# Optimization experiments

Hardware: AMD Instinct MI355X
Metric: run time of the kernel (lower is better)

## Reference

```python
import jax, jax.numpy as jnp
import numpy as np

B, D, O = 512, 256, 256
H = [512, 1024, 1024]

def _linear_params(key, fan_in, fan_out):
    kw, kb = jax.random.split(key)
    bound = 1.0 / np.sqrt(fan_in)
    W = jax.random.uniform(kw, (fan_out, fan_in), jnp.float32, -bound, bound)
    b = jax.random.uniform(kb, (fan_out,), jnp.float32, -bound, bound)
    return W, b

def setup_inputs() -> dict:
    key = jax.random.key(0)
    ks = jax.random.split(key, 7)
    input_values = jax.random.normal(ks[0], (B, D), jnp.float32)
    nan_flag = jax.random.uniform(ks[1], (B, D), jnp.float32)
    W_in, b_in = _linear_params(ks[2], D, H[0])          # input_layer: nan_flag_dim -> H[0]
    W_h1, b_h1 = _linear_params(ks[3], H[0], H[1])        # hidden layer 1
    W_h2, b_h2 = _linear_params(ks[4], H[1], H[2])        # hidden layer 2
    W_d, b_d = _linear_params(ks[5], H[2], D * O)         # output_branch_dense
    W_b, b_b = _linear_params(ks[6], H[2], O)             # output_branch_bias
    return {"input_values": input_values, "nan_flag": nan_flag, "training": False,
            "W_in": W_in, "b_in": b_in, "W_h1": W_h1, "b_h1": b_h1,
            "W_h2": W_h2, "b_h2": b_h2, "W_d": W_d, "b_d": b_d,
            "W_b": W_b, "b_b": b_b}

def reference(input_values, nan_flag, training, W_in, b_in, W_h1, b_h1, W_h2, b_h2, W_d, b_d, W_b, b_b):
    # training=False: dropout is identity, sample_missing branch skipped (default False)
    x = jax.nn.relu(nan_flag @ W_in.T + b_in)
    x = jax.nn.relu(x @ W_h1.T + b_h1)
    x = jax.nn.relu(x @ W_h2.T + b_h2)
    # per-sample compensation weights [B, D, O] and bias [B, O]
    comp_w = (x @ W_d.T + b_d).reshape(B, D, O)
    comp_b = x @ W_b.T + b_b
    # baddbmm: [B,1,D] @ [B,D,O] + [B,1,O] -> squeeze -> [B,O]
    out = comp_b + jnp.einsum('bd,bdo->bo', input_values, comp_w)
    return out
```

## Files before the change

kernel.cpp:

```cpp
#include <hip/hip_runtime.h>
#include <hip/hip_bf16.h>

#define B_  512
#define D_  256
#define O_  256
#define H2_ 1024

typedef __attribute__((ext_vector_type(4))) float  f32x4;
typedef __attribute__((ext_vector_type(8))) short  short8;
typedef __attribute__((ext_vector_type(4))) short  short4v;

union S8u  { short4v v; unsigned u[2]; };
union S16u { short8  v; unsigned u[4]; };

__device__ __forceinline__ unsigned f32_bf16(float x) {
  unsigned u = __builtin_bit_cast(unsigned, x);
  return (u + 0x7fffu + ((u >> 16) & 1u)) >> 16;
}
__device__ __forceinline__ unsigned cvt_pk_bf16(float a, float b) {
  return f32_bf16(a) | (f32_bf16(b) << 16);
}

__device__ __forceinline__ void gl_lds16(const void* g, void* l) {
  __builtin_amdgcn_global_load_lds(
      (const __attribute__((address_space(1))) unsigned int*)g,
      (__attribute__((address_space(3))) unsigned int*)l, 16, 0, 0);
}

__global__ __launch_bounds__(256)
void wcvt(const float* __restrict__ src, ushort* __restrict__ dst, int n8) {
  int i = blockIdx.x * 256 + threadIdx.x;
  const int stride = gridDim.x * 256;
  for (; i < n8; i += stride) {
    const f32x4* p = (const f32x4*)(src + (size_t)i * 8);
    f32x4 a = p[0], b = p[1];
    S16u s;
    s.u[0] = cvt_pk_bf16(a.x, a.y);
    s.u[1] = cvt_pk_bf16(a.z, a.w);
    s.u[2] = cvt_pk_bf16(b.x, b.y);
    s.u[3] = cvt_pk_bf16(b.z, b.w);
    *(short8*)(dst + (size_t)i * 8) = s.v;
  }
}

template <int RELU>
__global__ __launch_bounds__(256)
void gemm_bt64(const float* __restrict__ A, const float* __restrict__ Bm,
               const float* __restrict__ bias, float* __restrict__ C,
               int M, int N, int K) {
  __shared__ __align__(16) short As[64][72];
  __shared__ __align__(16) short Bs[64][72];
  const int t    = threadIdx.x;
  const int m0   = blockIdx.y * 64;
  const int n0   = blockIdx.x * 64;
  const int f4c  = t & 15;
  const int rg   = t >> 4;
  const int lane = t & 63;
  const int w    = t >> 6;
  const int wm   = (w & 1) * 32;
  const int wn   = (w >> 1) * 32;
  const int lr   = lane & 15;
  const int lq   = lane >> 4;

  f32x4 acc[2][2];
  #pragma unroll
  for (int i = 0; i < 2; ++i)
    #pragma unroll
    for (int j = 0; j < 2; ++j) acc[i][j] = f32x4{0.f, 0.f, 0.f, 0.f};

  for (int k0 = 0; k0 < K; k0 += 64) {
    #pragma unroll
    for (int j = 0; j < 4; ++j) {
      int r = rg + 16 * j;
      f32x4 av = *(const f32x4*)(A  + (size_t)(m0 + r) * K + k0 + f4c * 4);
      f32x4 bv = *(const f32x4*)(Bm + (size_t)(n0 + r) * K + k0 + f4c * 4);
      S8u sa; sa.u[0] = cvt_pk_bf16(av.x, av.y); sa.u[1] = cvt_pk_bf16(av.z, av.w);
      S8u sb; sb.u[0] = cvt_pk_bf16(bv.x, bv.y); sb.u[1] = cvt_pk_bf16(bv.z, bv.w);
      *(short4v*)&As[r][f4c * 4] = sa.v;
      *(short4v*)&Bs[r][f4c * 4] = sb.v;
    }
    __syncthreads();
    #pragma unroll
    for (int ks = 0; ks < 2; ++ks) {
      short8 a0 = *(const short8*)&As[wm + lr     ][ks * 32 + lq * 8];
      short8 a1 = *(const short8*)&As[wm + 16 + lr][ks * 32 + lq * 8];
      short8 b0 = *(const short8*)&Bs[wn + lr     ][ks * 32 + lq * 8];
      short8 b1 = *(const short8*)&Bs[wn + 16 + lr][ks * 32 + lq * 8];
      acc[0][0] = __builtin_amdgcn_mfma_f32_16x16x32_bf16(a0, b0, acc[0][0], 0, 0, 0);
      acc[0][1] = __builtin_amdgcn_mfma_f32_16x16x32_bf16(a0, b1, acc[0][1], 0, 0, 0);
      acc[1][0] = __builtin_amdgcn_mfma_f32_16x16x32_bf16(a1, b0, acc[1][0], 0, 0, 0);
      acc[1][1] = __builtin_amdgcn_mfma_f32_16x16x32_bf16(a1, b1, acc[1][1], 0, 0, 0);
    }
    __syncthreads();
  }
  #pragma unroll
  for (int mi = 0; mi < 2; ++mi)
    #pragma unroll
    for (int ni = 0; ni < 2; ++ni)
      #pragma unroll
      for (int r = 0; r < 4; ++r) {
        int row = m0 + wm + mi * 16 + lq * 4 + r;
        int col = n0 + wn + ni * 16 + lr;
        float v = acc[mi][ni][r] + bias[col];
        if (RELU) v = fmaxf(v, 0.f);
        C[(size_t)row * N + col] = v;
      }
}

__global__ __launch_bounds__(256)
void bias_d_kernel(const float* __restrict__ inp, const float* __restrict__ b_d,
                   float* __restrict__ out) {
  const int b = blockIdx.x;
  const int o = threadIdx.x;
  const float* ir = inp + (size_t)b * D_;
  float s = 0.f;
  #pragma unroll 8
  for (int d = 0; d < D_; ++d)
    s += ir[d] * b_d[(size_t)d * O_ + o];
  out[(size_t)b * O_ + o] += s;
}

__global__ __launch_bounds__(256)
void stage_b3(const float* __restrict__ x2, const float* __restrict__ inp,
              const ushort* __restrict__ Wdb, float* __restrict__ out) {
  __shared__ __align__(16) short  As[128][72];
  __shared__ __align__(16) ushort Bs[128 * 64];
  const int t    = threadIdx.x;
  const int mt   = blockIdx.x >> 1;
  const int nt   = blockIdx.x & 1;
  const int d0   = blockIdx.y * 4;
  const int bm   = mt * 128;
  const int bn   = nt * 128;
  const int f4c  = t & 15;
  const int rg   = t >> 4;
  const int lane = t & 63;
  const int w    = t >> 6;
  const int wm   = (w & 1) * 64;
  const int wn   = (w >> 1) * 64;
  const int lr   = lane & 15;
  const int lq   = lane >> 4;
  const int srow = t >> 3;
  const int skc  = (t & 7) ^ ((t >> 3) & 7);

  f32x4 acc[4][4];
  #pragma unroll
  for (int mi = 0; mi < 4; ++mi)
    #pragma unroll
    for (int ni = 0; ni < 4; ++ni) acc[mi][ni] = f32x4{0.f, 0.f, 0.f, 0.f};

  for (int dl = 0; dl < 4; ++dl) {
    const int d = d0 + dl;
    float insc[8];
    #pragma unroll
    for (int j = 0; j < 8; ++j)
      insc[j] = inp[(size_t)(bm + rg + 16 * j) * D_ + d];
    const ushort* wb = Wdb + ((size_t)d * O_ + bn) * H2_;

    for (int h0 = 0; h0 < H2_; h0 += 64) {
      #pragma unroll
      for (int r = 0; r < 4; ++r) {
        int n = r * 32 + srow;
        gl_lds16(wb + (size_t)n * H2_ + h0 + skc * 8, &Bs[(size_t)(r * 256 + t) * 8]);
      }
      #pragma unroll
      for (int j = 0; j < 8; ++j) {
        int rrow = rg + 16 * j;
        f32x4 xv = *(const f32x4*)(x2 + (size_t)(bm + rrow) * H2_ + h0 + f4c * 4);
        float s = insc[j];
        S8u sa;
        sa.u[0] = cvt_pk_bf16(xv.x * s, xv.y * s);
        sa.u[1] = cvt_pk_bf16(xv.z * s, xv.w * s);
        *(short4v*)&As[rrow][f4c * 4] = sa.v;
      }
      __syncthreads();
      #pragma unroll
      for (int ks = 0; ks < 2; ++ks) {
        short8 af[4], bfr[4];
        #pragma unroll
        for (int mi = 0; mi < 4; ++mi)
          af[mi] = *(const short8*)&As[wm + mi * 16 + lr][ks * 32 + lq * 8];
        #pragma unroll
        for (int ni = 0; ni < 4; ++ni) {
          int n  = wn + ni * 16 + lr;
          int kc = (ks * 4 + lq) ^ (n & 7);
          bfr[ni] = *(const short8*)&Bs[(size_t)(n * 8 + kc) * 8];
        }
        #pragma unroll
        for (int mi = 0; mi < 4; ++mi)
          #pragma unroll
          for (int ni = 0; ni < 4; ++ni)
            acc[mi][ni] = __builtin_amdgcn_mfma_f32_16x16x32_bf16(af[mi], bfr[ni],
                                                                  acc[mi][ni], 0, 0, 0);
      }
      __syncthreads();
    }
  }

  #pragma unroll
  for (int mi = 0; mi < 4; ++mi)
    #pragma unroll
    for (int ni = 0; ni < 4; ++ni)
      #pragma unroll
      for (int r = 0; r < 4; ++r) {
        int row = bm + wm + mi * 16 + lq * 4 + r;
        int col = bn + wn + ni * 16 + lr;
        atomicAdd(out + (size_t)row * O_ + col, acc[mi][ni][r]);
      }
}

__global__ __launch_bounds__(256, 2)
void stage_b(const float* __restrict__ x2, const float* __restrict__ inp,
             const float* __restrict__ Wd, float* __restrict__ out) {
  __shared__ __align__(16) short As[128][72];
  __shared__ __align__(16) short Bs[128][72];
  const int t    = threadIdx.x;
  const int mt   = blockIdx.x >> 1;
  const int nt   = blockIdx.x & 1;
  const int d0   = blockIdx.y * 4;
  const int bm   = mt * 128;
  const int bn   = nt * 128;
  const int f4c  = t & 15;
  const int rg   = t >> 4;
  const int lane = t & 63;
  const int w    = t >> 6;
  const int wm   = (w & 1) * 64;
  const int wn   = (w >> 1) * 64;
  const int lr   = lane & 15;
  const int lq   = lane >> 4;

  f32x4 acc[4][4];
  #pragma unroll
  for (int mi = 0; mi < 4; ++mi)
    #pragma unroll
    for (int ni = 0; ni < 4; ++ni) acc[mi][ni] = f32x4{0.f, 0.f, 0.f, 0.f};

  for (int dl = 0; dl < 4; ++dl) {
    const int d = d0 + dl;
    float insc[8];
    #pragma unroll
    for (int j = 0; j < 8; ++j)
      insc[j] = inp[(size_t)(bm + rg + 16 * j) * D_ + d];
    const float* wbase = Wd + ((size_t)d * O_ + bn) * H2_;

    for (int h0 = 0; h0 < H2_; h0 += 64) {
      #pragma unroll
      for (int j = 0; j < 8; ++j) {
        int r = rg + 16 * j;
        f32x4 xv = *(const f32x4*)(x2 + (size_t)(bm + r) * H2_ + h0 + f4c * 4);
        float s = insc[j];
        S8u sa;
        sa.u[0] = cvt_pk_bf16(xv.x * s, xv.y * s);
        sa.u[1] = cvt_pk_bf16(xv.z * s, xv.w * s);
        *(short4v*)&As[r][f4c * 4] = sa.v;
        f32x4 wv = *(const f32x4*)(wbase + (size_t)r * H2_ + h0 + f4c * 4);
        S8u sb; sb.u[0] = cvt_pk_bf16(wv.x, wv.y); sb.u[1] = cvt_pk_bf16(wv.z, wv.w);
        *(short4v*)&Bs[r][f4c * 4] = sb.v;
      }
      __syncthreads();
      #pragma unroll
      for (int ks = 0; ks < 2; ++ks) {
        short8 af[4], bfr[4];
        #pragma unroll
        for (int mi = 0; mi < 4; ++mi)
          af[mi] = *(const short8*)&As[wm + mi * 16 + lr][ks * 32 + lq * 8];
        #pragma unroll
        for (int ni = 0; ni < 4; ++ni)
          bfr[ni] = *(const short8*)&Bs[wn + ni * 16 + lr][ks * 32 + lq * 8];
        #pragma unroll
        for (int mi = 0; mi < 4; ++mi)
          #pragma unroll
          for (int ni = 0; ni < 4; ++ni)
            acc[mi][ni] = __builtin_amdgcn_mfma_f32_16x16x32_bf16(af[mi], bfr[ni],
                                                                  acc[mi][ni], 0, 0, 0);
      }
      __syncthreads();
    }
  }

  #pragma unroll
  for (int mi = 0; mi < 4; ++mi)
    #pragma unroll
    for (int ni = 0; ni < 4; ++ni)
      #pragma unroll
      for (int r = 0; r < 4; ++r) {
        int row = bm + wm + mi * 16 + lq * 4 + r;
        int col = bn + wn + ni * 16 + lr;
        atomicAdd(out + (size_t)row * O_ + col, acc[mi][ni][r]);
      }
}

extern "C" void kernel_launch(void* const* d_in, const int* in_sizes, int n_in,
                              void* d_out, int out_size, void* d_ws, size_t ws_size,
                              hipStream_t stream) {
  const float* input = (const float*)d_in[0];
  const float* nanf  = (const float*)d_in[1];
  const float* W_in  = (const float*)d_in[3];
  const float* b_in  = (const float*)d_in[4];
  const float* W_h1  = (const float*)d_in[5];
  const float* b_h1  = (const float*)d_in[6];
  const float* W_h2  = (const float*)d_in[7];
  const float* b_h2  = (const float*)d_in[8];
  const float* W_d   = (const float*)d_in[9];
  const float* b_d   = (const float*)d_in[10];
  const float* W_b   = (const float*)d_in[11];
  const float* b_b   = (const float*)d_in[12];
  float* out = (float*)d_out;

  float* x0 = (float*)d_ws;
  float* x1 = x0 + 512 * 512;
  float* x2 = x1 + 512 * 1024;
  ushort* Wdb = (ushort*)(x2 + 512 * 1024);
  const size_t need = 5242880 + (size_t)65536 * 1024 * 2;
  const bool use_bf16_w = ws_size >= need;

  if (use_bf16_w)
    wcvt<<<8192, 256, 0, stream>>>(W_d, Wdb, 65536 * 1024 / 8);

  gemm_bt64<1><<<dim3(8, 8),  256, 0, stream>>>(nanf, W_in, b_in, x0, 512, 512, 256);
  gemm_bt64<1><<<dim3(16, 8), 256, 0, stream>>>(x0, W_h1, b_h1, x1, 512, 1024, 512);
  gemm_bt64<1><<<dim3(16, 8), 256, 0, stream>>>(x1, W_h2, b_h2, x2, 512, 1024, 1024);
  gemm_bt64<0><<<dim3(4, 8),  256, 0, stream>>>(x2, W_b, b_b, out, 512, 256, 1024);
  bias_d_kernel<<<512, 256, 0, stream>>>(input, b_d, out);

  if (use_bf16_w)
    stage_b3<<<dim3(8, 64), 256, 0, stream>>>(x2, input, Wdb, out);
  else
    stage_b<<<dim3(8, 64), 256, 0, stream>>>(x2, input, W_d, out);
}
```

Before: 645.0 us.

## Double-buffer W_d tiles in LDS and build A fragments directly from global

The main compensation-weight GEMM now double-buffers the bf16 W_d tile in shared memory, prefetching the next tile while MFMAs run on the current one, and needs only one barrier per iteration. The A operand (x2 scaled by the input value) is no longer staged through LDS. Each wave loads its fp32 rows straight from global memory, scales them, converts to bf16 in registers and feeds the MFMA. This removes the LDS A tile and a barrier per step, but adds redundant global loads of x2 across waves and more register pressure.

```diff
diff --git a/kernel.cpp b/kernel.cpp
--- a/kernel.cpp
+++ b/kernel.cpp
@@ -121,18 +121,15 @@
 }
 
 __global__ __launch_bounds__(256)
-void stage_b3(const float* __restrict__ x2, const float* __restrict__ inp,
+void stage_b5(const float* __restrict__ x2, const float* __restrict__ inp,
               const ushort* __restrict__ Wdb, float* __restrict__ out) {
-  __shared__ __align__(16) short  As[128][72];
-  __shared__ __align__(16) ushort Bs[128 * 64];
+  __shared__ __align__(16) ushort Bb[2][128 * 64];
   const int t    = threadIdx.x;
   const int mt   = blockIdx.x >> 1;
   const int nt   = blockIdx.x & 1;
   const int d0   = blockIdx.y * 4;
   const int bm   = mt * 128;
   const int bn   = nt * 128;
-  const int f4c  = t & 15;
-  const int rg   = t >> 4;
   const int lane = t & 63;
   const int w    = t >> 6;
   const int wm   = (w & 1) * 64;
@@ -148,51 +145,70 @@
     #pragma unroll
     for (int ni = 0; ni < 4; ++ni) acc[mi][ni] = f32x4{0.f, 0.f, 0.f, 0.f};
 
-  for (int dl = 0; dl < 4; ++dl) {
-    const int d = d0 + dl;
-    float insc[8];
-    #pragma unroll
-    for (int j = 0; j < 8; ++j)
-      insc[j] = inp[(size_t)(bm + rg + 16 * j) * D_ + d];
-    const ushort* wb = Wdb + ((size_t)d * O_ + bn) * H2_;
-
-    for (int h0 = 0; h0 < H2_; h0 += 64) {
+  {
+    const ushort* wb = Wdb + ((size_t)d0 * O_ + bn) * H2_;
+    #pragma unroll
+    for (int r = 0; r < 4; ++r) {
+      int n = r * 32 + srow;
+      gl_lds16(wb + (size_t)n * H2_ + skc * 8, &Bb[0][(size_t)(r * 256 + t) * 8]);
+    }
+  }
+
+  float insc[4];
+  for (int it = 0; it < 64; ++it) {
+    const int p  = it & 1;
+    const int d  = d0 + (it >> 4);
+    const int h0 = (it & 15) * 64;
+    if ((it & 15) == 0) {
+      #pragma unroll
+      for (int mi = 0; mi < 4; ++mi)
+        insc[mi] = inp[(size_t)(bm + wm + mi * 16 + lr) * D_ + d];
+    }
+    __syncthreads();
+    if (it < 63) {
+      const int itn = it + 1;
+      const int dn  = d0 + (itn >> 4);
+      const int hn  = (itn & 15) * 64;
+      const ushort* wbn = Wdb + ((size_t)dn * O_ + bn) * H2_;
       #pragma unroll
       for (int r = 0; r < 4; ++r) {
         int n = r * 32 + srow;
-        gl_lds16(wb + (size_t)n * H2_ + h0 + skc * 8, &Bs[(size_t)(r * 256 + t) * 8]);
-      }
-      #pragma unroll
-      for (int j = 0; j < 8; ++j) {
-        int rrow = rg + 16 * j;
-        f32x4 xv = *(const f32x4*)(x2 + (size_t)(bm + rrow) * H2_ + h0 + f4c * 4);
-        float s = insc[j];
-        S8u sa;
-        sa.u[0] = cvt_pk_bf16(xv.x * s, xv.y * s);
-        sa.u[1] = cvt_pk_bf16(xv.z * s, xv.w * s);
-        *(short4v*)&As[rrow][f4c * 4] = sa.v;
-      }
-      __syncthreads();
-      #pragma unroll
-      for (int ks = 0; ks < 2; ++ks) {
-        short8 af[4], bfr[4];
-        #pragma unroll
-        for (int mi = 0; mi < 4; ++mi)
-          af[mi] = *(const short8*)&As[wm + mi * 16 + lr][ks * 32 + lq * 8];
+        gl_lds16(wbn + (size_t)n * H2_ + hn + skc * 8,
+                 &Bb[1 - p][(size_t)(r * 256 + t) * 8]);
+      }
+    }
+    #pragma unroll
+    for (int ks = 0; ks < 2; ++ks) {
+      short8 bfr[4];
+      #pragma unroll
+      for (int ni = 0; ni < 4; ++ni) {
+        int n  = wn + ni * 16 + lr;
+        int kc = (ks * 4 + lq) ^ (n & 7);
+        bfr[ni] = *(const short8*)&Bb[p][(size_t)(n * 8 + kc) * 8];
+      }
+      #pragma unroll
+      for (int mh = 0; mh < 2; ++mh) {
+        const int m0i = mh * 2;
+        const float* xp0 = x2 + (size_t)(bm + wm + m0i * 16 + lr) * H2_ + h0 + ks * 32 + lq * 8;
+        const float* xp1 = x2 + (size_t)(bm + wm + (m0i + 1) * 16 + lr) * H2_ + h0 + ks * 32 + lq * 8;
+        f32x4 x0a = *(const f32x4*)xp0, x0b = *(const f32x4*)(xp0 + 4);
+        f32x4 x1a = *(const f32x4*)xp1, x1b = *(const f32x4*)(xp1 + 4);
+        float s0 = insc[m0i], s1 = insc[m0i + 1];
+        S16u a0, a1;
+        a0.u[0] = cvt_pk_bf16(x0a.x * s0, x0a.y * s0);
+        a0.u[1] = cvt_pk_bf16(x0a.z * s0, x0a.w * s0);
+        a0.u[2] = cvt_pk_bf16(x0b.x * s0, x0b.y * s0);
+        a0.u[3] = cvt_pk_bf16(x0b.z * s0, x0b.w * s0);
+        a1.u[0] = cvt_pk_bf16(x1a.x * s1, x1a.y * s1);
+        a1.u[1] = cvt_pk_bf16(x1a.z * s1, x1a.w * s1);
+        a1.u[2] = cvt_pk_bf16(x1b.x * s1, x1b.y * s1);
+        a1.u[3] = cvt_pk_bf16(x1b.z * s1, x1b.w * s1);
         #pragma unroll
         for (int ni = 0; ni < 4; ++ni) {
-          int n  = wn + ni * 16 + lr;
-          int kc = (ks * 4 + lq) ^ (n & 7);
-          bfr[ni] = *(const short8*)&Bs[(size_t)(n * 8 + kc) * 8];
+          acc[m0i][ni]     = __builtin_amdgcn_mfma_f32_16x16x32_bf16(a0.v, bfr[ni], acc[m0i][ni],     0, 0, 0);
+          acc[m0i + 1][ni] = __builtin_amdgcn_mfma_f32_16x16x32_bf16(a1.v, bfr[ni], acc[m0i + 1][ni], 0, 0, 0);
         }
-        #pragma unroll
-        for (int mi = 0; mi < 4; ++mi)
-          #pragma unroll
-          for (int ni = 0; ni < 4; ++ni)
-            acc[mi][ni] = __builtin_amdgcn_mfma_f32_16x16x32_bf16(af[mi], bfr[ni],
-                                                                  acc[mi][ni], 0, 0, 0);
-      }
-      __syncthreads();
+      }
     }
   }
 
@@ -323,7 +339,7 @@
   bias_d_kernel<<<512, 256, 0, stream>>>(input, b_d, out);
 
   if (use_bf16_w)
-    stage_b3<<<dim3(8, 64), 256, 0, stream>>>(x2, input, Wdb, out);
+    stage_b5<<<dim3(8, 64), 256, 0, stream>>>(x2, input, Wdb, out);
   else
     stage_b<<<dim3(8, 64), 256, 0, stream>>>(x2, input, W_d, out);
 }
```

Result: slower. 793.2 us (+23.0%).

## Switch main contraction to fp16 with async LDS loads of pre-converted activations

Applied to the files above, without the earlier changes.

Converts W_d and x2 to fp16 in the workspace instead of bf16. The main kernel now loads the x2 tile straight into LDS with global_load_lds and applies the per-row input scale in registers before an fp16 MFMA. This removes the per-iteration fp32 global loads, scaling and bf16 packing from the inner loop. It adds an extra conversion kernel, a larger workspace requirement, and fp16 range/precision limits on the scaled activations.

```diff
diff --git a/kernel.cpp b/kernel.cpp
--- a/kernel.cpp
+++ b/kernel.cpp
@@ -6,12 +6,13 @@
 #define O_  256
 #define H2_ 1024
 
-typedef __attribute__((ext_vector_type(4))) float  f32x4;
-typedef __attribute__((ext_vector_type(8))) short  short8;
-typedef __attribute__((ext_vector_type(4))) short  short4v;
+typedef __attribute__((ext_vector_type(4))) float    f32x4;
+typedef __attribute__((ext_vector_type(8))) short    short8;
+typedef __attribute__((ext_vector_type(4))) short    short4v;
+typedef __attribute__((ext_vector_type(8))) _Float16 half8;
 
 union S8u  { short4v v; unsigned u[2]; };
-union S16u { short8  v; unsigned u[4]; };
+union H8u  { half8 v; short8 s; };
 
 __device__ __forceinline__ unsigned f32_bf16(float x) {
   unsigned u = __builtin_bit_cast(unsigned, x);
@@ -28,18 +29,16 @@
 }
 
 __global__ __launch_bounds__(256)
-void wcvt(const float* __restrict__ src, ushort* __restrict__ dst, int n8) {
+void wcvt_h(const float* __restrict__ src, _Float16* __restrict__ dst, int n8) {
   int i = blockIdx.x * 256 + threadIdx.x;
   const int stride = gridDim.x * 256;
   for (; i < n8; i += stride) {
     const f32x4* p = (const f32x4*)(src + (size_t)i * 8);
     f32x4 a = p[0], b = p[1];
-    S16u s;
-    s.u[0] = cvt_pk_bf16(a.x, a.y);
-    s.u[1] = cvt_pk_bf16(a.z, a.w);
-    s.u[2] = cvt_pk_bf16(b.x, b.y);
-    s.u[3] = cvt_pk_bf16(b.z, b.w);
-    *(short8*)(dst + (size_t)i * 8) = s.v;
+    half8 h;
+    h[0] = (_Float16)a.x; h[1] = (_Float16)a.y; h[2] = (_Float16)a.z; h[3] = (_Float16)a.w;
+    h[4] = (_Float16)b.x; h[5] = (_Float16)b.y; h[6] = (_Float16)b.z; h[7] = (_Float16)b.w;
+    *(half8*)(dst + (size_t)i * 8) = h;
   }
 }
 
@@ -121,9 +120,9 @@
 }
 
 __global__ __launch_bounds__(256)
-void stage_b3(const float* __restrict__ x2, const float* __restrict__ inp,
-              const ushort* __restrict__ Wdb, float* __restrict__ out) {
-  __shared__ __align__(16) short  As[128][72];
+void stage_b6(const _Float16* __restrict__ x2h, const float* __restrict__ inp,
+              const _Float16* __restrict__ Wdh, float* __restrict__ out) {
+  __shared__ __align__(16) ushort As[128 * 64];
   __shared__ __align__(16) ushort Bs[128 * 64];
   const int t    = threadIdx.x;
   const int mt   = blockIdx.x >> 1;
@@ -131,8 +130,6 @@
   const int d0   = blockIdx.y * 4;
   const int bm   = mt * 128;
   const int bn   = nt * 128;
-  const int f4c  = t & 15;
-  const int rg   = t >> 4;
   const int lane = t & 63;
   const int w    = t >> 6;
   const int wm   = (w & 1) * 64;
@@ -148,49 +145,47 @@
     #pragma unroll
     for (int ni = 0; ni < 4; ++ni) acc[mi][ni] = f32x4{0.f, 0.f, 0.f, 0.f};
 
+  const _Float16* xa = x2h + (size_t)bm * H2_;
+
   for (int dl = 0; dl < 4; ++dl) {
     const int d = d0 + dl;
-    float insc[8];
-    #pragma unroll
-    for (int j = 0; j < 8; ++j)
-      insc[j] = inp[(size_t)(bm + rg + 16 * j) * D_ + d];
-    const ushort* wb = Wdb + ((size_t)d * O_ + bn) * H2_;
+    const _Float16* wb = Wdh + ((size_t)d * O_ + bn) * H2_;
+    _Float16 hs[4];
+    #pragma unroll
+    for (int mi = 0; mi < 4; ++mi)
+      hs[mi] = (_Float16)inp[(size_t)(bm + wm + mi * 16 + lr) * D_ + d];
 
     for (int h0 = 0; h0 < H2_; h0 += 64) {
       #pragma unroll
       for (int r = 0; r < 4; ++r) {
         int n = r * 32 + srow;
+        gl_lds16(xa + (size_t)n * H2_ + h0 + skc * 8, &As[(size_t)(r * 256 + t) * 8]);
         gl_lds16(wb + (size_t)n * H2_ + h0 + skc * 8, &Bs[(size_t)(r * 256 + t) * 8]);
       }
-      #pragma unroll
-      for (int j = 0; j < 8; ++j) {
-        int rrow = rg + 16 * j;
-        f32x4 xv = *(const f32x4*)(x2 + (size_t)(bm + rrow) * H2_ + h0 + f4c * 4);
-        float s = insc[j];
-        S8u sa;
-        sa.u[0] = cvt_pk_bf16(xv.x * s, xv.y * s);
-        sa.u[1] = cvt_pk_bf16(xv.z * s, xv.w * s);
-        *(short4v*)&As[rrow][f4c * 4] = sa.v;
-      }
       __syncthreads();
       #pragma unroll
       for (int ks = 0; ks < 2; ++ks) {
-        short8 af[4], bfr[4];
-        #pragma unroll
-        for (int mi = 0; mi < 4; ++mi)
-          af[mi] = *(const short8*)&As[wm + mi * 16 + lr][ks * 32 + lq * 8];
+        half8 af[4], bfr[4];
+        #pragma unroll
+        for (int mi = 0; mi < 4; ++mi) {
+          int m  = wm + mi * 16 + lr;
+          int kc = (ks * 4 + lq) ^ (lr & 7);
+          af[mi] = *(const half8*)&As[(size_t)(m * 8 + kc) * 8];
+        }
         #pragma unroll
         for (int ni = 0; ni < 4; ++ni) {
           int n  = wn + ni * 16 + lr;
-          int kc = (ks * 4 + lq) ^ (n & 7);
-          bfr[ni] = *(const short8*)&Bs[(size_t)(n * 8 + kc) * 8];
+          int kc = (ks * 4 + lq) ^ (lr & 7);
+          bfr[ni] = *(const half8*)&Bs[(size_t)(n * 8 + kc) * 8];
         }
         #pragma unroll
-        for (int mi = 0; mi < 4; ++mi)
+        for (int mi = 0; mi < 4; ++mi) {
+          half8 asb = af[mi] * hs[mi];
           #pragma unroll
           for (int ni = 0; ni < 4; ++ni)
-            acc[mi][ni] = __builtin_amdgcn_mfma_f32_16x16x32_bf16(af[mi], bfr[ni],
-                                                                  acc[mi][ni], 0, 0, 0);
+            acc[mi][ni] = __builtin_amdgcn_mfma_f32_16x16x32_f16(asb, bfr[ni],
+                                                                 acc[mi][ni], 0, 0, 0);
+        }
       }
       __syncthreads();
     }
@@ -309,12 +304,13 @@
   float* x0 = (float*)d_ws;
   float* x1 = x0 + 512 * 512;
   float* x2 = x1 + 512 * 1024;
-  ushort* Wdb = (ushort*)(x2 + 512 * 1024);
-  const size_t need = 5242880 + (size_t)65536 * 1024 * 2;
-  const bool use_bf16_w = ws_size >= need;
-
-  if (use_bf16_w)
-    wcvt<<<8192, 256, 0, stream>>>(W_d, Wdb, 65536 * 1024 / 8);
+  _Float16* Wdh = (_Float16*)(x2 + 512 * 1024);
+  _Float16* x2h = Wdh + (size_t)65536 * 1024;
+  const size_t need = 5242880 + ((size_t)65536 * 1024 + 512 * 1024) * 2;
+  const bool use_f16 = ws_size >= need;
+
+  if (use_f16)
+    wcvt_h<<<8192, 256, 0, stream>>>(W_d, Wdh, 65536 * 1024 / 8);
 
   gemm_bt64<1><<<dim3(8, 8),  256, 0, stream>>>(nanf, W_in, b_in, x0, 512, 512, 256);
   gemm_bt64<1><<<dim3(16, 8), 256, 0, stream>>>(x0, W_h1, b_h1, x1, 512, 1024, 512);
@@ -322,8 +318,10 @@
   gemm_bt64<0><<<dim3(4, 8),  256, 0, stream>>>(x2, W_b, b_b, out, 512, 256, 1024);
   bias_d_kernel<<<512, 256, 0, stream>>>(input, b_d, out);
 
-  if (use_bf16_w)
-    stage_b3<<<dim3(8, 64), 256, 0, stream>>>(x2, input, Wdb, out);
-  else
+  if (use_f16) {
+    wcvt_h<<<256, 256, 0, stream>>>(x2, x2h, 512 * 1024 / 8);
+    stage_b6<<<dim3(8, 64), 256, 0, stream>>>(x2h, input, Wdh, out);
+  } else {
     stage_b<<<dim3(8, 64), 256, 0, stream>>>(x2, input, W_d, out);
-}
+  }
+}
```

New measurement: 640.8 us. No clear change (-0.6%).
